# Kernel tuning notes

Measured on AMD Instinct MI355X. Metric: run time of the kernel, lower is better.

Reference implementation:

```python
import jax, jax.numpy as jnp
import numpy as np

K = 64  # target active features per sample

def setup_inputs() -> dict:
    key = jax.random.key(0)
    x = jax.random.normal(key, (4096, 24576), dtype=jnp.float32)
    return {"x": x}

def reference(x) -> jnp.ndarray:
    # Training-mode BatchTopK: global threshold = min of top (k * batch) values
    # over the flattened batch, then ReLU(x) gated by (x >= threshold).
    batch_size = x.shape[0]
    total_k = min(K * batch_size, x.size)
    flat = x.reshape(-1)
    topv, _ = jax.lax.top_k(flat, total_k)
    threshold = jax.lax.stop_gradient(topv[-1])  # min of the top-k values (sorted desc)
    return jax.nn.relu(x) * (x >= threshold).astype(x.dtype)
```

## Files before the change

### kernel.cpp

```cpp
#include <hip/hip_runtime.h>

namespace {

struct SelState {
    unsigned forced_fb;
    unsigned bufcount;
    unsigned overflow;
    unsigned sel0;
    unsigned k1;
    unsigned sel1;
    unsigned k2;
};

constexpr int BINS12 = 4096;
constexpr int BINS8  = 256;
constexpr int LCAP   = 2048;
constexpr float GUESS = 2.5f;

using f4v = __attribute__((ext_vector_type(4))) float;

__device__ __forceinline__ unsigned f2key(float f) {
    unsigned u = __float_as_uint(f);
    return (u & 0x80000000u) ? ~u : (u | 0x80000000u);
}
__device__ __forceinline__ float key2f(unsigned k) {
    return __uint_as_float((k & 0x80000000u) ? (k & 0x7fffffffu) : ~k);
}
__device__ __forceinline__ bool is_fb(const SelState* st, unsigned total_k) {
    return st->forced_fb || st->overflow || (st->bufcount < total_k);
}

template <int NB>
__device__ __forceinline__ void scan_desc(const unsigned* __restrict__ hist, unsigned k,
                                          unsigned* __restrict__ lh, unsigned* __restrict__ res) {
    constexpr int CH = NB / 256;
    const int t = threadIdx.x;
    if (t == 0) { res[0] = 0; res[1] = k; }
    unsigned s = 0;
#pragma unroll
    for (int j = 0; j < CH; ++j) {
        unsigned c = hist[NB - 1 - (t * CH + j)];
        lh[t * CH + j] = c;
        s += c;
    }
    __syncthreads();
    const int lane = t & 63, wid = t >> 6;
    unsigned v = s;
#pragma unroll
    for (int d = 1; d < 64; d <<= 1) {
        unsigned u = __shfl_up(v, (unsigned)d, 64);
        if (lane >= d) v += u;
    }
    __shared__ unsigned wp[4];
    if (lane == 63) wp[wid] = v;
    __syncthreads();
    unsigned add = 0;
    for (int w = 0; w < wid; ++w) add += wp[w];
    v += add;
    unsigned pre = v - s;
    if (k > pre && k <= v) {
        unsigned cum = pre;
#pragma unroll
        for (int j = 0; j < CH; ++j) {
            unsigned c = lh[t * CH + j];
            if (cum + c >= k) { res[0] = (unsigned)(NB - 1 - (t * CH + j)); res[1] = k - cum; break; }
            cum += c;
        }
    }
    __syncthreads();
}

__global__ void init_kernel(unsigned* __restrict__ hist0s, unsigned* __restrict__ hist0f,
                            unsigned* __restrict__ hist1, unsigned* __restrict__ hist2,
                            SelState* __restrict__ st, unsigned force_fb) {
    int t = blockIdx.x * blockDim.x + threadIdx.x;
    int stride = gridDim.x * blockDim.x;
    for (int i = t; i < BINS12; i += stride) { hist0s[i] = 0; hist0f[i] = 0; hist1[i] = 0; }
    if (t < BINS8) hist2[t] = 0;
    if (t == 0) {
        st->forced_fb = force_fb;
        st->bufcount = 0;
        st->overflow = 0;
    }
}

__global__ __launch_bounds__(256) void pass1_kernel(const float* __restrict__ x, long long n,
                                                    unsigned* __restrict__ keys,
                                                    unsigned* __restrict__ idxs,
                                                    unsigned bufcap,
                                                    unsigned* __restrict__ hist0s,
                                                    SelState* __restrict__ st) {
    if (st->forced_fb) return;
    __shared__ unsigned lkey[LCAP];
    __shared__ unsigned lidx[LCAP];
    __shared__ unsigned lhist[BINS12];
    __shared__ unsigned lcnt;
    __shared__ unsigned gbase;
    for (int i = threadIdx.x; i < BINS12; i += 256) lhist[i] = 0;
    if (threadIdx.x == 0) lcnt = 0;
    __syncthreads();

    const unsigned GKEY = f2key(GUESS);
    long long n4 = n >> 2;
    long long tid = (long long)blockIdx.x * blockDim.x + threadIdx.x;
    long long stride = (long long)gridDim.x * blockDim.x;
    const f4v* xv = (const f4v*)x;

    for (long long i = tid; i < n4; i += stride) {
        f4v v = __builtin_nontemporal_load(&xv[i]);
#pragma unroll
        for (int c = 0; c < 4; ++c) {
            unsigned key = f2key(v[c]);
            if (key >= GKEY) {
                unsigned p = atomicAdd(&lcnt, 1u);
                if (p < LCAP) { lkey[p] = key; lidx[p] = (unsigned)((i << 2) + c); }
                atomicAdd(&lhist[key >> 20], 1u);
            }
        }
    }
    for (long long i = (n4 << 2) + tid; i < n; i += stride) {
        unsigned key = f2key(x[i]);
        if (key >= GKEY) {
            unsigned p = atomicAdd(&lcnt, 1u);
            if (p < LCAP) { lkey[p] = key; lidx[p] = (unsigned)i; }
            atomicAdd(&lhist[key >> 20], 1u);
        }
    }

    __syncthreads();
    unsigned cnt = lcnt;
    if (cnt > LCAP) cnt = LCAP;
    if (threadIdx.x == 0) {
        if (lcnt > LCAP) atomicOr(&st->overflow, 1u);
        unsigned base = atomicAdd(&st->bufcount, cnt);
        if (base + cnt > bufcap) atomicOr(&st->overflow, 1u);
        gbase = base;
    }
    __syncthreads();
    unsigned base = gbase;
    for (unsigned i = threadIdx.x; i < cnt; i += 256) {
        unsigned dst = base + i;
        if (dst < bufcap) { keys[dst] = lkey[i]; idxs[dst] = lidx[i]; }
    }
    for (int i = threadIdx.x; i < BINS12; i += 256) {
        unsigned c = lhist[i];
        if (c) atomicAdd(&hist0s[i], c);
    }
}

__global__ __launch_bounds__(256) void fb_hist0_kernel(const float* __restrict__ x, long long n,
                                                       unsigned* __restrict__ hist0f,
                                                       const SelState* __restrict__ st,
                                                       unsigned total_k) {
    if (!is_fb(st, total_k)) return;
    __shared__ unsigned lh[BINS12];
    for (int i = threadIdx.x; i < BINS12; i += 256) lh[i] = 0;
    __syncthreads();
    long long n4 = n >> 2;
    long long tid = (long long)blockIdx.x * blockDim.x + threadIdx.x;
    long long stride = (long long)gridDim.x * blockDim.x;
    const float4* x4 = (const float4*)x;
    for (long long i = tid; i < n4; i += stride) {
        float4 v = x4[i];
        float vv[4] = {v.x, v.y, v.z, v.w};
#pragma unroll
        for (int c = 0; c < 4; ++c) atomicAdd(&lh[f2key(vv[c]) >> 20], 1u);
    }
    for (long long i = (n4 << 2) + tid; i < n; i += stride)
        atomicAdd(&lh[f2key(x[i]) >> 20], 1u);
    __syncthreads();
    for (int i = threadIdx.x; i < BINS12; i += 256) {
        unsigned c = lh[i];
        if (c) atomicAdd(&hist0f[i], c);
    }
}

__global__ __launch_bounds__(256) void hist1_kernel(const float* __restrict__ x, long long n,
                                                    const unsigned* __restrict__ keys,
                                                    const unsigned* __restrict__ hist0s,
                                                    const unsigned* __restrict__ hist0f,
                                                    unsigned* __restrict__ hist1,
                                                    SelState* __restrict__ st,
                                                    unsigned total_k) {
    __shared__ unsigned lh[BINS12];
    __shared__ unsigned res[2];
    const bool fb = is_fb(st, total_k);
    scan_desc<BINS12>(fb ? hist0f : hist0s, total_k, lh, res);
    const unsigned sel0 = res[0];
    if (threadIdx.x == 0 && blockIdx.x == 0) { st->sel0 = sel0; st->k1 = res[1]; }

    for (int i = threadIdx.x; i < BINS12; i += 256) lh[i] = 0;
    __syncthreads();

    long long tid = (long long)blockIdx.x * blockDim.x + threadIdx.x;
    long long stride = (long long)gridDim.x * blockDim.x;

    if (fb) {
        long long n4 = n >> 2;
        const float4* x4 = (const float4*)x;
        for (long long i = tid; i < n4; i += stride) {
            float4 v = x4[i];
            float vv[4] = {v.x, v.y, v.z, v.w};
#pragma unroll
            for (int c = 0; c < 4; ++c) {
                unsigned key = f2key(vv[c]);
                if ((key >> 20) == sel0) atomicAdd(&lh[(key >> 8) & 0xFFFu], 1u);
            }
        }
        for (long long i = (n4 << 2) + tid; i < n; i += stride) {
            unsigned key = f2key(x[i]);
            if ((key >> 20) == sel0) atomicAdd(&lh[(key >> 8) & 0xFFFu], 1u);
        }
    } else {
        long long cnt = (long long)st->bufcount;
        long long c4 = cnt >> 2;
        const uint4* k4 = (const uint4*)keys;
        for (long long i = tid; i < c4; i += stride) {
            uint4 kv = k4[i];
            unsigned kk[4] = {kv.x, kv.y, kv.z, kv.w};
#pragma unroll
            for (int c = 0; c < 4; ++c)
                if ((kk[c] >> 20) == sel0) atomicAdd(&lh[(kk[c] >> 8) & 0xFFFu], 1u);
        }
        for (long long i = (c4 << 2) + tid; i < cnt; i += stride) {
            unsigned key = keys[i];
            if ((key >> 20) == sel0) atomicAdd(&lh[(key >> 8) & 0xFFFu], 1u);
        }
    }

    __syncthreads();
    for (int i = threadIdx.x; i < BINS12; i += 256) {
        unsigned c = lh[i];
        if (c) atomicAdd(&hist1[i], c);
    }
}

__global__ __launch_bounds__(256) void hist2_kernel(const float* __restrict__ x, long long n,
                                                    const unsigned* __restrict__ keys,
                                                    const unsigned* __restrict__ hist1,
                                                    unsigned* __restrict__ hist2,
                                                    SelState* __restrict__ st,
                                                    unsigned total_k) {
    __shared__ unsigned lh[BINS12];
    __shared__ unsigned res[2];
    scan_desc<BINS12>(hist1, st->k1, lh, res);
    const unsigned sel1 = (st->sel0 << 12) | res[0];
    if (threadIdx.x == 0 && blockIdx.x == 0) { st->sel1 = sel1; st->k2 = res[1]; }

    for (int i = threadIdx.x; i < BINS8; i += 256) lh[i] = 0;
    __syncthreads();

    long long tid = (long long)blockIdx.x * blockDim.x + threadIdx.x;
    long long stride = (long long)gridDim.x * blockDim.x;

    if (is_fb(st, total_k)) {
        long long n4 = n >> 2;
        const float4* x4 = (const float4*)x;
        for (long long i = tid; i < n4; i += stride) {
            float4 v = x4[i];
            float vv[4] = {v.x, v.y, v.z, v.w};
#pragma unroll
            for (int c = 0; c < 4; ++c) {
                unsigned key = f2key(vv[c]);
                if ((key >> 8) == sel1) atomicAdd(&lh[key & 0xFFu], 1u);
            }
        }
        for (long long i = (n4 << 2) + tid; i < n; i += stride) {
            unsigned key = f2key(x[i]);
            if ((key >> 8) == sel1) atomicAdd(&lh[key & 0xFFu], 1u);
        }
    } else {
        long long cnt = (long long)st->bufcount;
        long long c4 = cnt >> 2;
        const uint4* k4 = (const uint4*)keys;
        for (long long i = tid; i < c4; i += stride) {
            uint4 kv = k4[i];
            unsigned kk[4] = {kv.x, kv.y, kv.z, kv.w};
#pragma unroll
            for (int c = 0; c < 4; ++c)
                if ((kk[c] >> 8) == sel1) atomicAdd(&lh[kk[c] & 0xFFu], 1u);
        }
        for (long long i = (c4 << 2) + tid; i < cnt; i += stride) {
            unsigned key = keys[i];
            if ((key >> 8) == sel1) atomicAdd(&lh[key & 0xFFu], 1u);
        }
    }

    __syncthreads();
    for (int i = threadIdx.x; i < BINS8; i += 256) {
        unsigned c = lh[i];
        if (c) atomicAdd(&hist2[i], c);
    }
}

__global__ __launch_bounds__(256) void gate_kernel(const float* __restrict__ x,
                                                   float* __restrict__ out, long long n,
                                                   const unsigned* __restrict__ keys,
                                                   const unsigned* __restrict__ idxs,
                                                   const unsigned* __restrict__ hist2,
                                                   const SelState* __restrict__ st,
                                                   unsigned total_k) {
    __shared__ unsigned lh[BINS8];
    __shared__ unsigned res[2];
    scan_desc<BINS8>(hist2, st->k2, lh, res);
    const unsigned tkey = (st->sel1 << 8) | res[0];

    long long tid = (long long)blockIdx.x * blockDim.x + threadIdx.x;
    long long stride = (long long)gridDim.x * blockDim.x;

    if (is_fb(st, total_k)) {
        float thr = key2f(tkey);
        long long n4 = n >> 2;
        const float4* x4 = (const float4*)x;
        float4* o4 = (float4*)out;
        for (long long i = tid; i < n4; i += stride) {
            float4 v = x4[i];
            float4 r;
            r.x = (v.x >= thr) ? fmaxf(v.x, 0.f) : 0.f;
            r.y = (v.y >= thr) ? fmaxf(v.y, 0.f) : 0.f;
            r.z = (v.z >= thr) ? fmaxf(v.z, 0.f) : 0.f;
            r.w = (v.w >= thr) ? fmaxf(v.w, 0.f) : 0.f;
            o4[i] = r;
        }
        for (long long i = (n4 << 2) + tid; i < n; i += stride) {
            float v = x[i];
            out[i] = (v >= thr) ? fmaxf(v, 0.f) : 0.f;
        }
    } else {
        long long cnt = (long long)st->bufcount;
        for (long long i = tid; i < cnt; i += stride) {
            unsigned kk = keys[i];
            if (kk >= tkey) out[idxs[i]] = key2f(kk);
        }
    }
}

}

extern "C" void kernel_launch(void* const* d_in, const int* in_sizes, int n_in,
                              void* d_out, int out_size, void* d_ws, size_t ws_size,
                              hipStream_t stream) {
    const float* x = (const float*)d_in[0];
    float* out = (float*)d_out;
    long long n = (long long)in_sizes[0];

    long long tk = 64LL * 4096LL;
    if (tk > n) tk = n;
    unsigned total_k = (unsigned)tk;

    char* ws = (char*)d_ws;
    unsigned* hist0s = (unsigned*)(ws);
    unsigned* hist0f = (unsigned*)(ws + 16384);
    unsigned* hist1  = (unsigned*)(ws + 32768);
    unsigned* hist2  = (unsigned*)(ws + 49152);
    SelState* st     = (SelState*)(ws + 50176);

    unsigned bufcap = 0;
    unsigned* keys = (unsigned*)(ws + 65536);
    unsigned* idxs = nullptr;
    if (ws_size > 65536) {
        size_t avail = (ws_size - 65536) / 8;
        size_t cap = avail > 16u * 1024u * 1024u ? 16u * 1024u * 1024u : avail;
        bufcap = (unsigned)(cap & ~3ull);
        idxs = keys + bufcap;
    }
    unsigned force_fb = (bufcap < 2u * total_k || n > 0xFFFF0000LL) ? 1u : 0u;

    const int blocks = 2048;

    hipMemsetAsync(out, 0, (size_t)n * sizeof(float), stream);
    init_kernel<<<16, 256, 0, stream>>>(hist0s, hist0f, hist1, hist2, st, force_fb);
    pass1_kernel<<<blocks, 256, 0, stream>>>(x, n, keys, idxs, bufcap, hist0s, st);
    fb_hist0_kernel<<<blocks, 256, 0, stream>>>(x, n, hist0f, st, total_k);
    hist1_kernel<<<blocks, 256, 0, stream>>>(x, n, keys, hist0s, hist0f, hist1, st, total_k);
    hist2_kernel<<<blocks, 256, 0, stream>>>(x, n, keys, hist1, hist2, st, total_k);
    gate_kernel<<<blocks, 256, 0, stream>>>(x, out, n, keys, idxs, hist2, st, total_k);
}
```

Baseline: 211.5 us.

## Fuse output zeroing into pass1 and drop init kernel and memset

The full-size output memset is removed. Instead, pass1 writes zeros to the output with nontemporal stores while it streams the input, so the write overlaps the read pass. The init kernel is replaced by a small memset of the workspace header, and force_fb becomes a kernel argument rather than state read from memory. The pass1 shared histogram is cut to only the bins at or above the guess threshold, which lowers LDS use and init cost. The fallback path still works because the fallback gate writes every output element.

Result: faster. 201.4 us, median of 2 (-4.8%).

```diff
diff --git a/kernel.cpp b/kernel.cpp
--- a/kernel.cpp
+++ b/kernel.cpp
@@ -3,7 +3,6 @@
 namespace {
 
 struct SelState {
-    unsigned forced_fb;
     unsigned bufcount;
     unsigned overflow;
     unsigned sel0;
@@ -16,6 +15,8 @@
 constexpr int BINS8  = 256;
 constexpr int LCAP   = 2048;
 constexpr float GUESS = 2.5f;
+constexpr unsigned GBIN = 0xC02u;
+constexpr int CBINS = 0x1000 - 0xC02;
 
 using f4v = __attribute__((ext_vector_type(4))) float;
 
@@ -26,8 +27,8 @@
 __device__ __forceinline__ float key2f(unsigned k) {
     return __uint_as_float((k & 0x80000000u) ? (k & 0x7fffffffu) : ~k);
 }
-__device__ __forceinline__ bool is_fb(const SelState* st, unsigned total_k) {
-    return st->forced_fb || st->overflow || (st->bufcount < total_k);
+__device__ __forceinline__ bool is_fb(const SelState* st, unsigned total_k, unsigned force_fb) {
+    return force_fb || st->overflow || (st->bufcount < total_k);
 }
 
 template <int NB>
@@ -70,33 +71,20 @@
     __syncthreads();
 }
 
-__global__ void init_kernel(unsigned* __restrict__ hist0s, unsigned* __restrict__ hist0f,
-                            unsigned* __restrict__ hist1, unsigned* __restrict__ hist2,
-                            SelState* __restrict__ st, unsigned force_fb) {
-    int t = blockIdx.x * blockDim.x + threadIdx.x;
-    int stride = gridDim.x * blockDim.x;
-    for (int i = t; i < BINS12; i += stride) { hist0s[i] = 0; hist0f[i] = 0; hist1[i] = 0; }
-    if (t < BINS8) hist2[t] = 0;
-    if (t == 0) {
-        st->forced_fb = force_fb;
-        st->bufcount = 0;
-        st->overflow = 0;
-    }
-}
-
-__global__ __launch_bounds__(256) void pass1_kernel(const float* __restrict__ x, long long n,
+__global__ __launch_bounds__(256) void pass1_kernel(const float* __restrict__ x,
+                                                    float* __restrict__ out, long long n,
                                                     unsigned* __restrict__ keys,
                                                     unsigned* __restrict__ idxs,
                                                     unsigned bufcap,
                                                     unsigned* __restrict__ hist0s,
-                                                    SelState* __restrict__ st) {
-    if (st->forced_fb) return;
+                                                    SelState* __restrict__ st,
+                                                    unsigned force_fb) {
+    if (force_fb) return;
     __shared__ unsigned lkey[LCAP];
     __shared__ unsigned lidx[LCAP];
-    __shared__ unsigned lhist[BINS12];
-    __shared__ unsigned lcnt;
-    __shared__ unsigned gbase;
-    for (int i = threadIdx.x; i < BINS12; i += 256) lhist[i] = 0;
+    __shared__ unsigned lhist[CBINS];
+    __shared__ unsigned lcnt, gbase;
+    for (int i = threadIdx.x; i < CBINS; i += 256) lhist[i] = 0;
     if (threadIdx.x == 0) lcnt = 0;
     __syncthreads();
 
@@ -105,31 +93,35 @@
     long long tid = (long long)blockIdx.x * blockDim.x + threadIdx.x;
     long long stride = (long long)gridDim.x * blockDim.x;
     const f4v* xv = (const f4v*)x;
+    f4v* ov = (f4v*)out;
+    f4v z4 = {0.f, 0.f, 0.f, 0.f};
 
     for (long long i = tid; i < n4; i += stride) {
         f4v v = __builtin_nontemporal_load(&xv[i]);
+        __builtin_nontemporal_store(z4, &ov[i]);
 #pragma unroll
         for (int c = 0; c < 4; ++c) {
             unsigned key = f2key(v[c]);
             if (key >= GKEY) {
                 unsigned p = atomicAdd(&lcnt, 1u);
                 if (p < LCAP) { lkey[p] = key; lidx[p] = (unsigned)((i << 2) + c); }
-                atomicAdd(&lhist[key >> 20], 1u);
+                atomicAdd(&lhist[(key >> 20) - GBIN], 1u);
             }
         }
     }
     for (long long i = (n4 << 2) + tid; i < n; i += stride) {
-        unsigned key = f2key(x[i]);
+        float v = x[i];
+        out[i] = 0.f;
+        unsigned key = f2key(v);
         if (key >= GKEY) {
             unsigned p = atomicAdd(&lcnt, 1u);
             if (p < LCAP) { lkey[p] = key; lidx[p] = (unsigned)i; }
-            atomicAdd(&lhist[key >> 20], 1u);
-        }
-    }
-
-    __syncthreads();
-    unsigned cnt = lcnt;
-    if (cnt > LCAP) cnt = LCAP;
+            atomicAdd(&lhist[(key >> 20) - GBIN], 1u);
+        }
+    }
+
+    __syncthreads();
+    unsigned cnt = lcnt > LCAP ? LCAP : lcnt;
     if (threadIdx.x == 0) {
         if (lcnt > LCAP) atomicOr(&st->overflow, 1u);
         unsigned base = atomicAdd(&st->bufcount, cnt);
@@ -142,17 +134,17 @@
         unsigned dst = base + i;
         if (dst < bufcap) { keys[dst] = lkey[i]; idxs[dst] = lidx[i]; }
     }
-    for (int i = threadIdx.x; i < BINS12; i += 256) {
+    for (int i = threadIdx.x; i < CBINS; i += 256) {
         unsigned c = lhist[i];
-        if (c) atomicAdd(&hist0s[i], c);
-    }
-}
-
-__global__ __launch_bounds__(256) void fb_hist0_kernel(const float* __restrict__ x, long long n,
-                                                       unsigned* __restrict__ hist0f,
-                                                       const SelState* __restrict__ st,
-                                                       unsigned total_k) {
-    if (!is_fb(st, total_k)) return;
+        if (c) atomicAdd(&hist0s[GBIN + i], c);
+    }
+}
+
+__global__ __launch_bounds__(256) void fbh0_kernel(const float* __restrict__ x, long long n,
+                                                   unsigned* __restrict__ hist0f,
+                                                   const SelState* __restrict__ st,
+                                                   unsigned total_k, unsigned force_fb) {
+    if (!is_fb(st, total_k, force_fb)) return;
     __shared__ unsigned lh[BINS12];
     for (int i = threadIdx.x; i < BINS12; i += 256) lh[i] = 0;
     __syncthreads();
@@ -181,10 +173,10 @@
                                                     const unsigned* __restrict__ hist0f,
                                                     unsigned* __restrict__ hist1,
                                                     SelState* __restrict__ st,
-                                                    unsigned total_k) {
+                                                    unsigned total_k, unsigned force_fb) {
     __shared__ unsigned lh[BINS12];
     __shared__ unsigned res[2];
-    const bool fb = is_fb(st, total_k);
+    const bool fb = is_fb(st, total_k, force_fb);
     scan_desc<BINS12>(fb ? hist0f : hist0s, total_k, lh, res);
     const unsigned sel0 = res[0];
     if (threadIdx.x == 0 && blockIdx.x == 0) { st->sel0 = sel0; st->k1 = res[1]; }
@@ -240,7 +232,7 @@
                                                     const unsigned* __restrict__ hist1,
                                                     unsigned* __restrict__ hist2,
                                                     SelState* __restrict__ st,
-                                                    unsigned total_k) {
+                                                    unsigned total_k, unsigned force_fb) {
     __shared__ unsigned lh[BINS12];
     __shared__ unsigned res[2];
     scan_desc<BINS12>(hist1, st->k1, lh, res);
@@ -253,7 +245,7 @@
     long long tid = (long long)blockIdx.x * blockDim.x + threadIdx.x;
     long long stride = (long long)gridDim.x * blockDim.x;
 
-    if (is_fb(st, total_k)) {
+    if (is_fb(st, total_k, force_fb)) {
         long long n4 = n >> 2;
         const float4* x4 = (const float4*)x;
         for (long long i = tid; i < n4; i += stride) {
@@ -299,7 +291,7 @@
                                                    const unsigned* __restrict__ idxs,
                                                    const unsigned* __restrict__ hist2,
                                                    const SelState* __restrict__ st,
-                                                   unsigned total_k) {
+                                                   unsigned total_k, unsigned force_fb) {
     __shared__ unsigned lh[BINS8];
     __shared__ unsigned res[2];
     scan_desc<BINS8>(hist2, st->k2, lh, res);
@@ -308,7 +300,7 @@
     long long tid = (long long)blockIdx.x * blockDim.x + threadIdx.x;
     long long stride = (long long)gridDim.x * blockDim.x;
 
-    if (is_fb(st, total_k)) {
+    if (is_fb(st, total_k, force_fb)) {
         float thr = key2f(tkey);
         long long n4 = n >> 2;
         const float4* x4 = (const float4*)x;
@@ -368,11 +360,10 @@
 
     const int blocks = 2048;
 
-    hipMemsetAsync(out, 0, (size_t)n * sizeof(float), stream);
-    init_kernel<<<16, 256, 0, stream>>>(hist0s, hist0f, hist1, hist2, st, force_fb);
-    pass1_kernel<<<blocks, 256, 0, stream>>>(x, n, keys, idxs, bufcap, hist0s, st);
-    fb_hist0_kernel<<<blocks, 256, 0, stream>>>(x, n, hist0f, st, total_k);
-    hist1_kernel<<<blocks, 256, 0, stream>>>(x, n, keys, hist0s, hist0f, hist1, st, total_k);
-    hist2_kernel<<<blocks, 256, 0, stream>>>(x, n, keys, hist1, hist2, st, total_k);
-    gate_kernel<<<blocks, 256, 0, stream>>>(x, out, n, keys, idxs, hist2, st, total_k);
-}
+    hipMemsetAsync(ws, 0, 50176 + sizeof(SelState), stream);
+    pass1_kernel<<<blocks, 256, 0, stream>>>(x, out, n, keys, idxs, bufcap, hist0s, st, force_fb);
+    fbh0_kernel<<<blocks, 256, 0, stream>>>(x, n, hist0f, st, total_k, force_fb);
+    hist1_kernel<<<blocks, 256, 0, stream>>>(x, n, keys, hist0s, hist0f, hist1, st, total_k, force_fb);
+    hist2_kernel<<<blocks, 256, 0, stream>>>(x, n, keys, hist1, hist2, st, total_k, force_fb);
+    gate_kernel<<<blocks, 256, 0, stream>>>(x, out, n, keys, idxs, hist2, st, total_k, force_fb);
+}
```
